# Performance work log

Measured on AMD Instinct MI355X. Metric: run time of the kernel, lower is better.

The kernel has to match this reference:

```python
import jax, jax.numpy as jnp
import numpy as np

V = 16384      # total nodes
G = 32         # nodes per graph (512 graphs)
D = 256        # node embedding dim == hidden_size
N = 8          # heads
H = 32         # head size
I = 1024       # intermediate size
LN_EPS = 1e-12


def _layer_norm(x, g, b):
    mu = jnp.mean(x, axis=-1, keepdims=True)
    var = jnp.mean(jnp.square(x - mu), axis=-1, keepdims=True)
    return (x - mu) * jax.lax.rsqrt(var + LN_EPS) * g + b


def setup_inputs() -> dict:
    key = jax.random.key(0)
    ks = jax.random.split(key, 5)
    node_embeddings = jax.random.normal(ks[0], (V, D), jnp.float32)
    # fully-connected pairs within each graph of size G (sorted by source node)
    idx = np.arange(V, dtype=np.int32).reshape(-1, G)          # [num_graphs, G]
    src = np.repeat(idx, G, axis=1).reshape(-1)                # [P]
    dst = np.tile(idx, (1, G)).reshape(-1)                     # [P]
    in_graph_node_pairs = jnp.asarray(np.stack([src, dst], axis=-1))  # [P, 2]
    s = 0.02
    return {
        "node_embeddings": node_embeddings,
        "in_graph_node_pairs": in_graph_node_pairs,
        "W_qkv": jax.random.normal(ks[1], (D, 3 * N * H), jnp.float32) * s,
        "W_o": jax.random.normal(ks[2], (N * H, D), jnp.float32) * s,
        "ln1_g": jnp.ones((D,), jnp.float32),
        "ln1_b": jnp.zeros((D,), jnp.float32),
        "W_i": jax.random.normal(ks[3], (D, I), jnp.float32) * s,
        "W_out2": jax.random.normal(ks[4], (I, D), jnp.float32) * s,
        "ln2_g": jnp.ones((D,), jnp.float32),
        "ln2_b": jnp.zeros((D,), jnp.float32),
    }


def reference(node_embeddings, in_graph_node_pairs, W_qkv, W_o, ln1_g, ln1_b,
              W_i, W_out2, ln2_g, ln2_b):
    nV = node_embeddings.shape[0]
    src = in_graph_node_pairs[:, 0]
    dst = in_graph_node_pairs[:, 1]
    # QKV projection -> [V, N, 3H] -> split
    qkv = (node_embeddings @ W_qkv).reshape(nV, N, 3 * H)
    q, k, v = jnp.split(qkv, 3, axis=-1)                       # each [V, N, H]
    # per-pair scores [P, N]
    scores = jnp.einsum('phi,phi->ph', q[src], k[dst]) / jnp.sqrt(jnp.float32(H))
    # segment softmax over source node, all heads at once
    m = jax.ops.segment_max(scores, src, num_segments=nV)       # [V, N]
    e = jnp.exp(scores - m[src])
    denom = jax.ops.segment_sum(e, src, num_segments=nV)        # [V, N]
    w = e / denom[src]                                          # [P, N]
    # weighted value scatter-sum -> [V, N, H]
    wv = w[:, :, None] * v[dst]
    att = jax.ops.segment_sum(wv, src, num_segments=nV).reshape(nV, N * H)
    # output projection + residual + LN
    pre = _layer_norm(att @ W_o + node_embeddings, ln1_g, ln1_b)
    inter = jax.nn.gelu(pre @ W_i, approximate=False)
    out = _layer_norm(inter @ W_out2 + pre, ln2_g, ln2_b)
    return out
```

## Files before the change

kernel.cpp:

```cpp
#include <hip/hip_runtime.h>
#include <math.h>

#define V 16384
#define D 256
#define NH 256
#define THREE_NH 768
#define IDIM 1024
#define LN_EPS 1e-12f

typedef short s16x8 __attribute__((ext_vector_type(8)));
typedef float f32x4 __attribute__((ext_vector_type(4)));

__device__ inline unsigned short f2bf(float f) {
    unsigned u = __float_as_uint(f);
    u += 0x7fffu + ((u >> 16) & 1u);
    return (unsigned short)(u >> 16);
}
__device__ inline float bf2f(unsigned short s) {
    return __uint_as_float(((unsigned)s) << 16);
}
__device__ inline float bflo(unsigned v) { return __uint_as_float(v << 16); }
__device__ inline float bfhi(unsigned v) { return __uint_as_float(v & 0xffff0000u); }

__device__ inline void gl2lds16(const unsigned short* g, unsigned short* l) {
    __builtin_amdgcn_global_load_lds(
        (__attribute__((address_space(1))) void*)(g),
        (__attribute__((address_space(3))) void*)(l), 16, 0, 0);
}

template <int ROWS_T>
__device__ inline void stage(const unsigned short* __restrict__ src, size_t row0,
                             int ldk, int k0, unsigned short* lds, int wv, int lane) {
    constexpr int PER_WAVE = ROWS_T / 32;
    #pragma unroll
    for (int i = 0; i < PER_WAVE; ++i) {
        const int seg = wv * PER_WAVE + i;
        const int r = seg * 8 + (lane >> 3);
        const int c = (lane & 7) ^ (r & 7);
        gl2lds16(src + (row0 + (size_t)r) * ldk + k0 + c * 8, lds + seg * 512);
    }
}

__device__ inline s16x8 fragld(const unsigned short* lds, int row, int chunk) {
    return *(const s16x8*)&lds[row * 64 + ((chunk ^ (row & 7)) << 3)];
}

__global__ __launch_bounds__(256) void prep(const float* __restrict__ X,
                                            unsigned short* __restrict__ Xb,
                                            const float* __restrict__ Wqkv,
                                            const float* __restrict__ Wo,
                                            const float* __restrict__ Wi,
                                            const float* __restrict__ Wo2,
                                            unsigned short* __restrict__ WqkvT,
                                            unsigned short* __restrict__ WoT,
                                            unsigned short* __restrict__ WiT,
                                            unsigned short* __restrict__ Wo2T) {
    const int b = blockIdx.x, t = threadIdx.x;
    if (b >= 768) {
        int i = (b - 768) * 256 + t;
        float4 v = ((const float4*)X)[i];
        ushort4 o;
        o.x = f2bf(v.x); o.y = f2bf(v.y); o.z = f2bf(v.z); o.w = f2bf(v.w);
        ((ushort4*)Xb)[i] = o;
        return;
    }
    __shared__ float tile[32][33];
    const float* W; unsigned short* Wt; int K, N, bx, by;
    if (b < 192)      { W = Wqkv; Wt = WqkvT; K = 256;  N = 768;  bx = b & 7;          by = b >> 3; }
    else if (b < 256) { W = Wo;   Wt = WoT;   K = 256;  N = 256;  bx = (b - 192) & 7;  by = (b - 192) >> 3; }
    else if (b < 512) { W = Wi;   Wt = WiT;   K = 256;  N = 1024; bx = (b - 256) & 7;  by = (b - 256) >> 3; }
    else              { W = Wo2;  Wt = Wo2T;  K = 1024; N = 256;  bx = (b - 512) & 31; by = (b - 512) >> 5; }
    const int k0 = bx * 32, n0 = by * 32;
    #pragma unroll
    for (int p = 0; p < 4; ++p) {
        int idx = t + p * 256, r = idx >> 5, c = idx & 31;
        tile[r][c] = W[(size_t)(k0 + r) * N + n0 + c];
    }
    __syncthreads();
    #pragma unroll
    for (int p = 0; p < 4; ++p) {
        int idx = t + p * 256, r = idx >> 5, c = idx & 31;
        Wt[(size_t)(n0 + r) * K + k0 + c] = f2bf(tile[c][r]);
    }
}

template <int K, int N, int EPI>
__global__ __launch_bounds__(256) void gemm128(const unsigned short* __restrict__ A,
                                               const unsigned short* __restrict__ Bt,
                                               unsigned short* __restrict__ C) {
    __shared__ unsigned short As[128 * 64];
    __shared__ unsigned short Bs[128 * 64];
    const int t = threadIdx.x;
    const int r0 = blockIdx.x * 128, c0 = blockIdx.y * 128;
    const int wv = t >> 6, lane = t & 63, q = lane >> 4, l16 = lane & 15;
    const int wr = (wv >> 1) * 64, wc = (wv & 1) * 64;
    f32x4 acc[4][4] = {};

    for (int k0 = 0; k0 < K; k0 += 64) {
        __syncthreads();
        stage<128>(A,  (size_t)r0, K, k0, As, wv, lane);
        stage<128>(Bt, (size_t)c0, K, k0, Bs, wv, lane);
        __builtin_amdgcn_s_waitcnt(0);
        __syncthreads();
        #pragma unroll
        for (int kk2 = 0; kk2 < 2; ++kk2) {
            s16x8 af[4], bfr[4];
            #pragma unroll
            for (int mf = 0; mf < 4; ++mf)
                af[mf] = fragld(As, wr + mf * 16 + l16, kk2 * 4 + q);
            #pragma unroll
            for (int nf = 0; nf < 4; ++nf)
                bfr[nf] = fragld(Bs, wc + nf * 16 + l16, kk2 * 4 + q);
            #pragma unroll
            for (int mf = 0; mf < 4; ++mf)
                #pragma unroll
                for (int nf = 0; nf < 4; ++nf)
                    acc[mf][nf] = __builtin_amdgcn_mfma_f32_16x16x32_bf16(af[mf], bfr[nf], acc[mf][nf], 0, 0, 0);
        }
    }

    #pragma unroll
    for (int mf = 0; mf < 4; ++mf)
        #pragma unroll
        for (int nf = 0; nf < 4; ++nf) {
            const int cg = c0 + wc + nf * 16 + l16;
            #pragma unroll
            for (int r = 0; r < 4; ++r) {
                const int rg = r0 + wr + mf * 16 + q * 4 + r;
                float v = acc[mf][nf][r];
                if (EPI == 1) v = 0.5f * v * (1.f + erff(v * 0.70710678118654752f));
                C[(size_t)rg * N + cg] = f2bf(v);
            }
        }
}

template <int K, bool OUTF, bool RESBF>
__global__ __launch_bounds__(256) void gemm_ln(const unsigned short* __restrict__ A,
                                               const unsigned short* __restrict__ Bt,
                                               const void* __restrict__ resv,
                                               const float* __restrict__ gamma,
                                               const float* __restrict__ beta,
                                               float* __restrict__ outf,
                                               unsigned short* __restrict__ outb) {
    __shared__ unsigned short As[32 * 64];
    __shared__ unsigned short Bs[256 * 64];
    __shared__ float2 partial[4][32];
    __shared__ float2 stats[32];
    const int t = threadIdx.x, r0 = blockIdx.x * 32;
    const int wv = t >> 6, lane = t & 63, q = lane >> 4, l16 = lane & 15;
    const int wc = wv * 64;
    f32x4 acc[2][4] = {};

    for (int k0 = 0; k0 < K; k0 += 64) {
        __syncthreads();
        stage<32>(A, (size_t)r0, K, k0, As, wv, lane);
        stage<256>(Bt, 0, K, k0, Bs, wv, lane);
        __builtin_amdgcn_s_waitcnt(0);
        __syncthreads();
        #pragma unroll
        for (int kk2 = 0; kk2 < 2; ++kk2) {
            s16x8 af[2], bfr[4];
            #pragma unroll
            for (int mf = 0; mf < 2; ++mf)
                af[mf] = fragld(As, mf * 16 + l16, kk2 * 4 + q);
            #pragma unroll
            for (int nf = 0; nf < 4; ++nf)
                bfr[nf] = fragld(Bs, wc + nf * 16 + l16, kk2 * 4 + q);
            #pragma unroll
            for (int mf = 0; mf < 2; ++mf)
                #pragma unroll
                for (int nf = 0; nf < 4; ++nf)
                    acc[mf][nf] = __builtin_amdgcn_mfma_f32_16x16x32_bf16(af[mf], bfr[nf], acc[mf][nf], 0, 0, 0);
        }
    }

    #pragma unroll
    for (int mf = 0; mf < 2; ++mf)
        #pragma unroll
        for (int nf = 0; nf < 4; ++nf) {
            const int cg = wc + nf * 16 + l16;
            #pragma unroll
            for (int r = 0; r < 4; ++r) {
                const size_t idx = (size_t)(r0 + mf * 16 + q * 4 + r) * NH + cg;
                float rv;
                if (RESBF) rv = bf2f(((const unsigned short*)resv)[idx]);
                else       rv = ((const float*)resv)[idx];
                acc[mf][nf][r] += rv;
            }
        }

    #pragma unroll
    for (int mf = 0; mf < 2; ++mf) {
        float s[4] = {0.f, 0.f, 0.f, 0.f}, ss[4] = {0.f, 0.f, 0.f, 0.f};
        #pragma unroll
        for (int nf = 0; nf < 4; ++nf)
            #pragma unroll
            for (int r = 0; r < 4; ++r) {
                float v = acc[mf][nf][r];
                s[r] += v; ss[r] += v * v;
            }
        #pragma unroll
        for (int off = 1; off < 16; off <<= 1)
            #pragma unroll
            for (int r = 0; r < 4; ++r) {
                s[r]  += __shfl_xor(s[r],  off);
                ss[r] += __shfl_xor(ss[r], off);
            }
        if (l16 == 0)
            #pragma unroll
            for (int r = 0; r < 4; ++r)
                partial[wv][mf * 16 + q * 4 + r] = make_float2(s[r], ss[r]);
    }
    __syncthreads();
    if (t < 32) {
        float s = 0.f, ss = 0.f;
        #pragma unroll
        for (int w = 0; w < 4; ++w) { s += partial[w][t].x; ss += partial[w][t].y; }
        float mu  = s * (1.f / 256.f);
        float var = ss * (1.f / 256.f) - mu * mu;
        stats[t] = make_float2(mu, rsqrtf(var + LN_EPS));
    }
    __syncthreads();

    #pragma unroll
    for (int mf = 0; mf < 2; ++mf)
        #pragma unroll
        for (int nf = 0; nf < 4; ++nf) {
            const int cg = wc + nf * 16 + l16;
            const float g = gamma[cg], b = beta[cg];
            #pragma unroll
            for (int r = 0; r < 4; ++r) {
                const int rl = mf * 16 + q * 4 + r;
                const float2 st = stats[rl];
                float v = (acc[mf][nf][r] - st.x) * st.y * g + b;
                const size_t idx = (size_t)(r0 + rl) * NH + cg;
                if (OUTF) outf[idx] = v;
                else      outb[idx] = f2bf(v);
            }
        }
}

#define LDR 776
__global__ __launch_bounds__(256) void attln(const unsigned short* __restrict__ qkv,
                                             const unsigned short* __restrict__ WoT,
                                             const float* __restrict__ X,
                                             const float* __restrict__ gamma,
                                             const float* __restrict__ beta,
                                             unsigned short* __restrict__ preb) {
    __shared__ unsigned short smem[33536 + 320];
    unsigned short* s  = smem;
    unsigned short* pt = smem + 24832;
    unsigned short* at = smem;
    unsigned short* Bs = smem + 8192;
    float2* partial = (float2*)(smem + 24832);
    float2* stats   = (float2*)(smem + 24832 + 512);

    const int g = blockIdx.x;
    const int t = threadIdx.x;
    const int h = t >> 5, u = t & 31;
    const int ub = u & 7;
    const int us = u >> 3;
    const int qc = h * 96;

    const unsigned short* src = qkv + (size_t)g * 32 * THREE_NH;
    #pragma unroll
    for (int pp = 0; pp < 12; ++pp) {
        int c = t + pp * 256;
        int row = c / 96, col8 = c % 96;
        s16x8 vv = *(const s16x8*)&src[c * 8];
        *(s16x8*)&s[row * LDR + col8 * 8] = vv;
    }
    __syncthreads();

    float sc[4][8];
    #pragma unroll
    for (int di = 0; di < 4; ++di)
        #pragma unroll
        for (int dj = 0; dj < 8; ++dj) sc[di][dj] = 0.f;

    for (int kq = 0; kq < 8; ++kq) {
        float qv[4][4];
        #pragma unroll
        for (int di = 0; di < 4; ++di) {
            uint2 v = *(const uint2*)&s[(ub + 8 * di) * LDR + qc + 4 * kq];
            qv[di][0] = bflo(v.x); qv[di][1] = bfhi(v.x);
            qv[di][2] = bflo(v.y); qv[di][3] = bfhi(v.y);
        }
        #pragma unroll
        for (int dj = 0; dj < 8; ++dj) {
            uint2 v = *(const uint2*)&s[(us + 4 * dj) * LDR + qc + 32 + 4 * kq];
            float kv[4];
            kv[0] = bflo(v.x); kv[1] = bfhi(v.x);
            kv[2] = bflo(v.y); kv[3] = bfhi(v.y);
            #pragma unroll
            for (int di = 0; di < 4; ++di)
                #pragma unroll
                for (int kk = 0; kk < 4; ++kk)
                    sc[di][dj] = fmaf(qv[di][kk], kv[kk], sc[di][dj]);
        }
    }

    #pragma unroll
    for (int di = 0; di < 4; ++di) {
        float m = sc[di][0];
        #pragma unroll
        for (int dj = 1; dj < 8; ++dj) m = fmaxf(m, sc[di][dj]);
        m = fmaxf(m, __shfl_xor(m, 8));
        m = fmaxf(m, __shfl_xor(m, 16));
        float sum = 0.f;
        #pragma unroll
        for (int dj = 0; dj < 8; ++dj) {
            float e = __expf((sc[di][dj] - m) * 0.17677669529663687f);
            sc[di][dj] = e;
            sum += e;
        }
        sum += __shfl_xor(sum, 8);
        sum += __shfl_xor(sum, 16);
        float inv = 1.f / sum;
        const int rb = h * 1088 + (ub + 8 * di) * 34;
        #pragma unroll
        for (int dj = 0; dj < 8; ++dj)
            pt[rb + us + 4 * dj] = f2bf(sc[di][dj] * inv);
    }
    __syncthreads();

    const int vc = qc + 64, d0 = us * 8;
    float o[4][8];
    #pragma unroll
    for (int di = 0; di < 4; ++di)
        #pragma unroll
        for (int dd = 0; dd < 8; ++dd) o[di][dd] = 0.f;

    for (int j = 0; j < 32; ++j) {
        float pv[4];
        #pragma unroll
        for (int di = 0; di < 4; ++di)
            pv[di] = bf2f(pt[h * 1088 + (ub + 8 * di) * 34 + j]);
        #pragma unroll
        for (int dq = 0; dq < 2; ++dq) {
            uint2 v = *(const uint2*)&s[j * LDR + vc + d0 + 4 * dq];
            float v0 = bflo(v.x), v1 = bfhi(v.x), v2 = bflo(v.y), v3 = bfhi(v.y);
            #pragma unroll
            for (int di = 0; di < 4; ++di) {
                o[di][dq * 4 + 0] = fmaf(pv[di], v0, o[di][dq * 4 + 0]);
                o[di][dq * 4 + 1] = fmaf(pv[di], v1, o[di][dq * 4 + 1]);
                o[di][dq * 4 + 2] = fmaf(pv[di], v2, o[di][dq * 4 + 2]);
                o[di][dq * 4 + 3] = fmaf(pv[di], v3, o[di][dq * 4 + 3]);
            }
        }
    }
    __syncthreads();

    {
        const int col = h * 32 + d0;
        const int kb = col >> 6, c = (col & 63) >> 3;
        #pragma unroll
        for (int di = 0; di < 4; ++di) {
            const int i = ub + 8 * di;
            s16x8 ov;
            #pragma unroll
            for (int dd = 0; dd < 8; ++dd) ov[dd] = (short)f2bf(o[di][dd]);
            *(s16x8*)&at[kb * 2048 + i * 64 + ((c ^ (i & 7)) << 3)] = ov;
        }
    }

    const int wv = t >> 6, lane = t & 63, q = lane >> 4, l16 = lane & 15;
    const int wc = wv * 64;
    const int r0 = g * 32;
    f32x4 acc[2][4] = {};

    for (int k0 = 0; k0 < 256; k0 += 64) {
        __syncthreads();
        stage<256>(WoT, 0, 256, k0, Bs, wv, lane);
        __builtin_amdgcn_s_waitcnt(0);
        __syncthreads();
        const unsigned short* atk = at + (k0 >> 6) * 2048;
        #pragma unroll
        for (int kk2 = 0; kk2 < 2; ++kk2) {
            s16x8 af[2], bfr[4];
            #pragma unroll
            for (int mf = 0; mf < 2; ++mf)
                af[mf] = fragld(atk, mf * 16 + l16, kk2 * 4 + q);
            #pragma unroll
            for (int nf = 0; nf < 4; ++nf)
                bfr[nf] = fragld(Bs, wc + nf * 16 + l16, kk2 * 4 + q);
            #pragma unroll
            for (int mf = 0; mf < 2; ++mf)
                #pragma unroll
                for (int nf = 0; nf < 4; ++nf)
                    acc[mf][nf] = __builtin_amdgcn_mfma_f32_16x16x32_bf16(af[mf], bfr[nf], acc[mf][nf], 0, 0, 0);
        }
    }

    #pragma unroll
    for (int mf = 0; mf < 2; ++mf)
        #pragma unroll
        for (int nf = 0; nf < 4; ++nf) {
            const int cg = wc + nf * 16 + l16;
            #pragma unroll
            for (int r = 0; r < 4; ++r)
                acc[mf][nf][r] += X[(size_t)(r0 + mf * 16 + q * 4 + r) * NH + cg];
        }

    #pragma unroll
    for (int mf = 0; mf < 2; ++mf) {
        float sp[4] = {0.f, 0.f, 0.f, 0.f}, ssp[4] = {0.f, 0.f, 0.f, 0.f};
        #pragma unroll
        for (int nf = 0; nf < 4; ++nf)
            #pragma unroll
            for (int r = 0; r < 4; ++r) {
                float v = acc[mf][nf][r];
                sp[r] += v; ssp[r] += v * v;
            }
        #pragma unroll
        for (int off = 1; off < 16; off <<= 1)
            #pragma unroll
            for (int r = 0; r < 4; ++r) {
                sp[r]  += __shfl_xor(sp[r],  off);
                ssp[r] += __shfl_xor(ssp[r], off);
            }
        if (l16 == 0)
            #pragma unroll
            for (int r = 0; r < 4; ++r)
                partial[wv * 32 + mf * 16 + q * 4 + r] = make_float2(sp[r], ssp[r]);
    }
    __syncthreads();
    if (t < 32) {
        float sv = 0.f, ssv = 0.f;
        #pragma unroll
        for (int w = 0; w < 4; ++w) { sv += partial[w * 32 + t].x; ssv += partial[w * 32 + t].y; }
        float mu  = sv * (1.f / 256.f);
        float var = ssv * (1.f / 256.f) - mu * mu;
        stats[t] = make_float2(mu, rsqrtf(var + LN_EPS));
    }
    __syncthreads();

    #pragma unroll
    for (int mf = 0; mf < 2; ++mf)
        #pragma unroll
        for (int nf = 0; nf < 4; ++nf) {
            const int cg = wc + nf * 16 + l16;
            const float gm = gamma[cg], bt = beta[cg];
            #pragma unroll
            for (int r = 0; r < 4; ++r) {
                const int rl = mf * 16 + q * 4 + r;
                const float2 st = stats[rl];
                float v = (acc[mf][nf][r] - st.x) * st.y * gm + bt;
                preb[(size_t)(r0 + rl) * NH + cg] = f2bf(v);
            }
        }
}

extern "C" void kernel_launch(void* const* d_in, const int* in_sizes, int n_in,
                              void* d_out, int out_size, void* d_ws, size_t ws_size,
                              hipStream_t stream) {
    const float* X      = (const float*)d_in[0];
    const float* W_qkv  = (const float*)d_in[2];
    const float* W_o    = (const float*)d_in[3];
    const float* ln1_g  = (const float*)d_in[4];
    const float* ln1_b  = (const float*)d_in[5];
    const float* W_i    = (const float*)d_in[6];
    const float* W_out2 = (const float*)d_in[7];
    const float* ln2_g  = (const float*)d_in[8];
    const float* ln2_b  = (const float*)d_in[9];
    float* out = (float*)d_out;

    char* ws = (char*)d_ws;
    unsigned short* Xbf   = (unsigned short*)(ws);
    unsigned short* qkvb  = (unsigned short*)(ws + 8388608);
    unsigned short* preb  = (unsigned short*)(ws + 58720256);
    unsigned short* WqkvT = (unsigned short*)(ws + 67108864);
    unsigned short* WoT   = (unsigned short*)(ws + 67502080);
    unsigned short* WiT   = (unsigned short*)(ws + 67633152);
    unsigned short* Wo2T  = (unsigned short*)(ws + 68157440);
    unsigned short* interb = (unsigned short*)(ws);

    dim3 blk(256);
    hipLaunchKernelGGL(prep, dim3(768 + V * D / 4 / 256), blk, 0, stream,
                       X, Xbf, W_qkv, W_o, W_i, W_out2, WqkvT, WoT, WiT, Wo2T);

    hipLaunchKernelGGL((gemm128<D, THREE_NH, 0>), dim3(V / 128, THREE_NH / 128), blk, 0, stream,
                       Xbf, WqkvT, qkvb);
    hipLaunchKernelGGL(attln, dim3(V / 32), blk, 0, stream,
                       qkvb, WoT, X, ln1_g, ln1_b, preb);
    hipLaunchKernelGGL((gemm128<D, IDIM, 1>), dim3(V / 128, IDIM / 128), blk, 0, stream,
                       preb, WiT, interb);
    hipLaunchKernelGGL((gemm_ln<IDIM, true, true>), dim3(V / 32), blk, 0, stream,
                       interb, Wo2T, (const void*)preb, ln2_g, ln2_b, out, (unsigned short*)nullptr);
}
```

Before: 166.5 us.

## Stream weight fragments from global memory and stage only activations in LDS

The GEMM kernels now keep the whole activation K-slab in LDS, loaded once, and read B (weight) MFMA fragments straight from global memory instead of staging them through LDS. Tiles widen to 128x256 for the QKV and FFN-up GEMMs, the final GEMM+LN uses 64-row blocks with double-buffered A chunks, and the attention kernel's Wo projection also loads weights directly. This is meant to cut LDS traffic and per-k-step barriers and rely on L2/L1 caching of the small weight matrices. The cost is more register pressure from wider accumulators and uncoalesced strided global loads for B fragments.

Measured after the change: 210.3 us. +26.4%, slower.

```diff
diff --git a/kernel.cpp b/kernel.cpp
--- a/kernel.cpp
+++ b/kernel.cpp
@@ -43,6 +43,11 @@
 
 __device__ inline s16x8 fragld(const unsigned short* lds, int row, int chunk) {
     return *(const s16x8*)&lds[row * 64 + ((chunk ^ (row & 7)) << 3)];
+}
+
+__device__ inline s16x8 bfrag(const unsigned short* __restrict__ Bt, int K,
+                              int nbase, int l16, int k0, int chunk) {
+    return *(const s16x8*)&Bt[(size_t)(nbase + l16) * K + k0 + (chunk << 3)];
 }
 
 __global__ __launch_bounds__(256) void prep(const float* __restrict__ X,
@@ -85,44 +90,45 @@
 }
 
 template <int K, int N, int EPI>
-__global__ __launch_bounds__(256) void gemm128(const unsigned short* __restrict__ A,
-                                               const unsigned short* __restrict__ Bt,
-                                               unsigned short* __restrict__ C) {
-    __shared__ unsigned short As[128 * 64];
-    __shared__ unsigned short Bs[128 * 64];
+__global__ __launch_bounds__(256, 2) void gemmW(const unsigned short* __restrict__ A,
+                                                const unsigned short* __restrict__ Bt,
+                                                unsigned short* __restrict__ C) {
+    __shared__ unsigned short As[128 * K];
     const int t = threadIdx.x;
-    const int r0 = blockIdx.x * 128, c0 = blockIdx.y * 128;
+    const int r0 = blockIdx.x * 128, c0 = blockIdx.y * 256;
     const int wv = t >> 6, lane = t & 63, q = lane >> 4, l16 = lane & 15;
-    const int wr = (wv >> 1) * 64, wc = (wv & 1) * 64;
-    f32x4 acc[4][4] = {};
-
-    for (int k0 = 0; k0 < K; k0 += 64) {
-        __syncthreads();
-        stage<128>(A,  (size_t)r0, K, k0, As, wv, lane);
-        stage<128>(Bt, (size_t)c0, K, k0, Bs, wv, lane);
-        __builtin_amdgcn_s_waitcnt(0);
-        __syncthreads();
+    const int wr = (wv >> 1) * 64, wc = (wv & 1) * 128;
+    f32x4 acc[4][8] = {};
+
+    #pragma unroll
+    for (int kc = 0; kc < K / 64; ++kc)
+        stage<128>(A, (size_t)r0, K, kc * 64, As + kc * 8192, wv, lane);
+    __builtin_amdgcn_s_waitcnt(0);
+    __syncthreads();
+
+    #pragma unroll
+    for (int kc = 0; kc < K / 64; ++kc) {
+        const unsigned short* Ak = As + kc * 8192;
         #pragma unroll
         for (int kk2 = 0; kk2 < 2; ++kk2) {
-            s16x8 af[4], bfr[4];
+            s16x8 af[4];
             #pragma unroll
             for (int mf = 0; mf < 4; ++mf)
-                af[mf] = fragld(As, wr + mf * 16 + l16, kk2 * 4 + q);
-            #pragma unroll
-            for (int nf = 0; nf < 4; ++nf)
-                bfr[nf] = fragld(Bs, wc + nf * 16 + l16, kk2 * 4 + q);
-            #pragma unroll
-            for (int mf = 0; mf < 4; ++mf)
+                af[mf] = fragld(Ak, wr + mf * 16 + l16, kk2 * 4 + q);
+            #pragma unroll
+            for (int nf = 0; nf < 8; ++nf) {
+                const s16x8 bv = bfrag(Bt, K, c0 + wc + nf * 16, l16, kc * 64, kk2 * 4 + q);
                 #pragma unroll
-                for (int nf = 0; nf < 4; ++nf)
-                    acc[mf][nf] = __builtin_amdgcn_mfma_f32_16x16x32_bf16(af[mf], bfr[nf], acc[mf][nf], 0, 0, 0);
+                for (int mf = 0; mf < 4; ++mf)
+                    acc[mf][nf] = __builtin_amdgcn_mfma_f32_16x16x32_bf16(af[mf], bv, acc[mf][nf], 0, 0, 0);
+            }
         }
     }
 
     #pragma unroll
     for (int mf = 0; mf < 4; ++mf)
         #pragma unroll
-        for (int nf = 0; nf < 4; ++nf) {
+        for (int nf = 0; nf < 8; ++nf) {
             const int cg = c0 + wc + nf * 16 + l16;
             #pragma unroll
             for (int r = 0; r < 4; ++r) {
@@ -134,63 +140,71 @@
         }
 }
 
-template <int K, bool OUTF, bool RESBF>
-__global__ __launch_bounds__(256) void gemm_ln(const unsigned short* __restrict__ A,
-                                               const unsigned short* __restrict__ Bt,
-                                               const void* __restrict__ resv,
-                                               const float* __restrict__ gamma,
-                                               const float* __restrict__ beta,
-                                               float* __restrict__ outf,
-                                               unsigned short* __restrict__ outb) {
-    __shared__ unsigned short As[32 * 64];
-    __shared__ unsigned short Bs[256 * 64];
-    __shared__ float2 partial[4][32];
-    __shared__ float2 stats[32];
-    const int t = threadIdx.x, r0 = blockIdx.x * 32;
+__global__ __launch_bounds__(256, 2) void gemm_wo2ln(const unsigned short* __restrict__ A,
+                                                     const unsigned short* __restrict__ Bt,
+                                                     const unsigned short* __restrict__ resb,
+                                                     const float* __restrict__ gamma,
+                                                     const float* __restrict__ beta,
+                                                     float* __restrict__ out) {
+    __shared__ unsigned short As[2][64 * 256];
+    __shared__ float2 partial[4][64];
+    __shared__ float2 stats[64];
+    const int t = threadIdx.x, r0 = blockIdx.x * 64;
     const int wv = t >> 6, lane = t & 63, q = lane >> 4, l16 = lane & 15;
     const int wc = wv * 64;
-    f32x4 acc[2][4] = {};
-
-    for (int k0 = 0; k0 < K; k0 += 64) {
+    f32x4 acc[4][4] = {};
+
+    #pragma unroll
+    for (int kc = 0; kc < 4; ++kc)
+        stage<64>(A, (size_t)r0, IDIM, kc * 64, As[0] + kc * 4096, wv, lane);
+
+    #pragma unroll
+    for (int ch = 0; ch < 4; ++ch) {
+        const unsigned short* Ac = As[ch & 1];
+        if (ch < 3) {
+            #pragma unroll
+            for (int kc = 0; kc < 4; ++kc)
+                stage<64>(A, (size_t)r0, IDIM, (ch + 1) * 256 + kc * 64,
+                          As[(ch & 1) ^ 1] + kc * 4096, wv, lane);
+            asm volatile("s_waitcnt vmcnt(8)" ::: "memory");
+        } else {
+            asm volatile("s_waitcnt vmcnt(0)" ::: "memory");
+        }
         __syncthreads();
-        stage<32>(A, (size_t)r0, K, k0, As, wv, lane);
-        stage<256>(Bt, 0, K, k0, Bs, wv, lane);
-        __builtin_amdgcn_s_waitcnt(0);
+        #pragma unroll
+        for (int kc = 0; kc < 4; ++kc) {
+            const unsigned short* Ak = Ac + kc * 4096;
+            const int kg = ch * 256 + kc * 64;
+            #pragma unroll
+            for (int kk2 = 0; kk2 < 2; ++kk2) {
+                s16x8 af[4];
+                #pragma unroll
+                for (int mf = 0; mf < 4; ++mf)
+                    af[mf] = fragld(Ak, mf * 16 + l16, kk2 * 4 + q);
+                #pragma unroll
+                for (int nf = 0; nf < 4; ++nf) {
+                    const s16x8 bv = bfrag(Bt, IDIM, wc + nf * 16, l16, kg, kk2 * 4 + q);
+                    #pragma unroll
+                    for (int mf = 0; mf < 4; ++mf)
+                        acc[mf][nf] = __builtin_amdgcn_mfma_f32_16x16x32_bf16(af[mf], bv, acc[mf][nf], 0, 0, 0);
+                }
+            }
+        }
         __syncthreads();
-        #pragma unroll
-        for (int kk2 = 0; kk2 < 2; ++kk2) {
-            s16x8 af[2], bfr[4];
-            #pragma unroll
-            for (int mf = 0; mf < 2; ++mf)
-                af[mf] = fragld(As, mf * 16 + l16, kk2 * 4 + q);
-            #pragma unroll
-            for (int nf = 0; nf < 4; ++nf)
-                bfr[nf] = fragld(Bs, wc + nf * 16 + l16, kk2 * 4 + q);
-            #pragma unroll
-            for (int mf = 0; mf < 2; ++mf)
-                #pragma unroll
-                for (int nf = 0; nf < 4; ++nf)
-                    acc[mf][nf] = __builtin_amdgcn_mfma_f32_16x16x32_bf16(af[mf], bfr[nf], acc[mf][nf], 0, 0, 0);
-        }
-    }
-
-    #pragma unroll
-    for (int mf = 0; mf < 2; ++mf)
+    }
+
+    #pragma unroll
+    for (int mf = 0; mf < 4; ++mf)
         #pragma unroll
         for (int nf = 0; nf < 4; ++nf) {
             const int cg = wc + nf * 16 + l16;
             #pragma unroll
-            for (int r = 0; r < 4; ++r) {
-                const size_t idx = (size_t)(r0 + mf * 16 + q * 4 + r) * NH + cg;
-                float rv;
-                if (RESBF) rv = bf2f(((const unsigned short*)resv)[idx]);
-                else       rv = ((const float*)resv)[idx];
-                acc[mf][nf][r] += rv;
-            }
-        }
-
-    #pragma unroll
-    for (int mf = 0; mf < 2; ++mf) {
+            for (int r = 0; r < 4; ++r)
+                acc[mf][nf][r] += bf2f(resb[(size_t)(r0 + mf * 16 + q * 4 + r) * NH + cg]);
+        }
+
+    #pragma unroll
+    for (int mf = 0; mf < 4; ++mf) {
         float s[4] = {0.f, 0.f, 0.f, 0.f}, ss[4] = {0.f, 0.f, 0.f, 0.f};
         #pragma unroll
         for (int nf = 0; nf < 4; ++nf)
@@ -212,18 +226,18 @@
                 partial[wv][mf * 16 + q * 4 + r] = make_float2(s[r], ss[r]);
     }
     __syncthreads();
-    if (t < 32) {
-        float s = 0.f, ss = 0.f;
-        #pragma unroll
-        for (int w = 0; w < 4; ++w) { s += partial[w][t].x; ss += partial[w][t].y; }
-        float mu  = s * (1.f / 256.f);
-        float var = ss * (1.f / 256.f) - mu * mu;
+    if (t < 64) {
+        float sv = 0.f, ssv = 0.f;
+        #pragma unroll
+        for (int w = 0; w < 4; ++w) { sv += partial[w][t].x; ssv += partial[w][t].y; }
+        float mu  = sv * (1.f / 256.f);
+        float var = ssv * (1.f / 256.f) - mu * mu;
         stats[t] = make_float2(mu, rsqrtf(var + LN_EPS));
     }
     __syncthreads();
 
     #pragma unroll
-    for (int mf = 0; mf < 2; ++mf)
+    for (int mf = 0; mf < 4; ++mf)
         #pragma unroll
         for (int nf = 0; nf < 4; ++nf) {
             const int cg = wc + nf * 16 + l16;
@@ -232,10 +246,7 @@
             for (int r = 0; r < 4; ++r) {
                 const int rl = mf * 16 + q * 4 + r;
                 const float2 st = stats[rl];
-                float v = (acc[mf][nf][r] - st.x) * st.y * g + b;
-                const size_t idx = (size_t)(r0 + rl) * NH + cg;
-                if (OUTF) outf[idx] = v;
-                else      outb[idx] = f2bf(v);
+                out[(size_t)(r0 + rl) * NH + cg] = (acc[mf][nf][r] - st.x) * st.y * g + b;
             }
         }
 }
@@ -251,7 +262,6 @@
     unsigned short* s  = smem;
     unsigned short* pt = smem + 24832;
     unsigned short* at = smem;
-    unsigned short* Bs = smem + 8192;
     float2* partial = (float2*)(smem + 24832);
     float2* stats   = (float2*)(smem + 24832 + 512);
 
@@ -363,32 +373,29 @@
             *(s16x8*)&at[kb * 2048 + i * 64 + ((c ^ (i & 7)) << 3)] = ov;
         }
     }
+    __syncthreads();
 
     const int wv = t >> 6, lane = t & 63, q = lane >> 4, l16 = lane & 15;
     const int wc = wv * 64;
     const int r0 = g * 32;
     f32x4 acc[2][4] = {};
 
-    for (int k0 = 0; k0 < 256; k0 += 64) {
-        __syncthreads();
-        stage<256>(WoT, 0, 256, k0, Bs, wv, lane);
-        __builtin_amdgcn_s_waitcnt(0);
-        __syncthreads();
-        const unsigned short* atk = at + (k0 >> 6) * 2048;
+    #pragma unroll
+    for (int kc = 0; kc < 4; ++kc) {
+        const unsigned short* atk = at + kc * 2048;
         #pragma unroll
         for (int kk2 = 0; kk2 < 2; ++kk2) {
-            s16x8 af[2], bfr[4];
+            s16x8 af[2];
             #pragma unroll
             for (int mf = 0; mf < 2; ++mf)
                 af[mf] = fragld(atk, mf * 16 + l16, kk2 * 4 + q);
             #pragma unroll
-            for (int nf = 0; nf < 4; ++nf)
-                bfr[nf] = fragld(Bs, wc + nf * 16 + l16, kk2 * 4 + q);
-            #pragma unroll
-            for (int mf = 0; mf < 2; ++mf)
+            for (int nf = 0; nf < 4; ++nf) {
+                const s16x8 bv = bfrag(WoT, NH, wc + nf * 16, l16, kc * 64, kk2 * 4 + q);
                 #pragma unroll
-                for (int nf = 0; nf < 4; ++nf)
-                    acc[mf][nf] = __builtin_amdgcn_mfma_f32_16x16x32_bf16(af[mf], bfr[nf], acc[mf][nf], 0, 0, 0);
+                for (int mf = 0; mf < 2; ++mf)
+                    acc[mf][nf] = __builtin_amdgcn_mfma_f32_16x16x32_bf16(af[mf], bv, acc[mf][nf], 0, 0, 0);
+            }
         }
     }
 
@@ -479,12 +486,12 @@
     hipLaunchKernelGGL(prep, dim3(768 + V * D / 4 / 256), blk, 0, stream,
                        X, Xbf, W_qkv, W_o, W_i, W_out2, WqkvT, WoT, WiT, Wo2T);
 
-    hipLaunchKernelGGL((gemm128<D, THREE_NH, 0>), dim3(V / 128, THREE_NH / 128), blk, 0, stream,
+    hipLaunchKernelGGL((gemmW<D, THREE_NH, 0>), dim3(V / 128, THREE_NH / 256), blk, 0, stream,
                        Xbf, WqkvT, qkvb);
     hipLaunchKernelGGL(attln, dim3(V / 32), blk, 0, stream,
                        qkvb, WoT, X, ln1_g, ln1_b, preb);
-    hipLaunchKernelGGL((gemm128<D, IDIM, 1>), dim3(V / 128, IDIM / 128), blk, 0, stream,
+    hipLaunchKernelGGL((gemmW<D, IDIM, 1>), dim3(V / 128, IDIM / 256), blk, 0, stream,
                        preb, WiT, interb);
-    hipLaunchKernelGGL((gemm_ln<IDIM, true, true>), dim3(V / 32), blk, 0, stream,
-                       interb, Wo2T, (const void*)preb, ln2_g, ln2_b, out, (unsigned short*)nullptr);
-}
+    hipLaunchKernelGGL(gemm_wo2ln, dim3(V / 64), blk, 0, stream,
+                       interb, Wo2T, preb, ln2_g, ln2_b, out);
+}
```
